# Optimization experiments

Hardware: AMD Instinct MI355X
Metric: run time of the kernel (lower is better)

The kernel has to match this reference:

```python
import jax, jax.numpy as jnp
import numpy as np

B, C, HH, WW = 16, 256, 64, 64
K, H, U, R = 16, 4, 4, 23
DIM_OUT = 256
DV = DIM_OUT // H  # 64
N = HH * WW
EPS = 1e-3  # keras BatchNormalization default epsilon


def setup_inputs() -> dict:
    key = jax.random.key(0)
    ks = jax.random.split(key, 16)
    sc = 0.02
    return {
        "x": jax.random.normal(ks[0], (B, C, HH, WW), jnp.float32),
        "w_q": jax.random.normal(ks[1], (K * H, C), jnp.float32) * sc,
        "w_k": jax.random.normal(ks[2], (K * U, C), jnp.float32) * sc,
        "w_v": jax.random.normal(ks[3], (DV * U, C), jnp.float32) * sc,
        "gamma_q": jnp.ones((K * H,), jnp.float32),
        "beta_q": jnp.zeros((K * H,), jnp.float32),
        "mean_q": jax.random.normal(ks[4], (K * H,), jnp.float32) * 0.1,
        "var_q": jax.random.uniform(ks[5], (K * H,), jnp.float32) + 0.5,
        "gamma_v": jnp.ones((DV * U,), jnp.float32),
        "beta_v": jnp.zeros((DV * U,), jnp.float32),
        "mean_v": jax.random.normal(ks[6], (DV * U,), jnp.float32) * 0.1,
        "var_v": jax.random.uniform(ks[7], (DV * U,), jnp.float32) + 0.5,
        "w_pos": jax.random.normal(ks[8], (K, U, 1, R, R), jnp.float32) * sc,
        "b_pos": jnp.zeros((K,), jnp.float32),
    }


def _bn(x, gamma, beta, mean, var):
    # inference-mode batchnorm over channel axis 1, x: [b,c,h,w]
    inv = gamma * jax.lax.rsqrt(var + EPS)
    return x * inv[None, :, None, None] + (beta - mean * inv)[None, :, None, None]


def reference(x, w_q, w_k, w_v, gamma_q, beta_q, mean_q, var_q,
              gamma_v, beta_v, mean_v, var_v, w_pos, b_pos):
    b = x.shape[0]
    # 1x1 conv projections (channels-first)
    q = jnp.einsum('oc,bchw->bohw', w_q, x)
    k = jnp.einsum('oc,bchw->bohw', w_k, x)
    v = jnp.einsum('oc,bchw->bohw', w_v, x)
    q = _bn(q, gamma_q, beta_q, mean_q, var_q)
    v = _bn(v, gamma_v, beta_v, mean_v, var_v)
    # rearrange to sequence form
    q = q.reshape(b, H, K, N)           # b h k n
    k = k.reshape(b, U, K, N)           # b u k m
    v = v.reshape(b, U, DV, N)          # b u v m
    k = jax.nn.softmax(k, axis=-1)      # softmax over positions m
    # content lambda
    Lc = jnp.einsum('bukm,buvm->bkv', k, v)
    Yc = jnp.einsum('bhkn,bkv->bnhv', q, Lc)
    # position lambda via local 3D conv over (v, hh, ww) with kernel (1, r, r)
    v5 = v.reshape(b, U, DV, HH, WW)
    Lp = jax.lax.conv_general_dilated(
        v5, w_pos, window_strides=(1, 1, 1),
        padding=[(0, 0), (R // 2, R // 2), (R // 2, R // 2)],
        dimension_numbers=('NCDHW', 'OIDHW', 'NCDHW'))
    Lp = Lp + b_pos[None, :, None, None, None]
    Lp = Lp.reshape(b, K, DV, N)        # b k v n
    Yp = jnp.einsum('bhkn,bkvn->bnhv', q, Lp)
    Y = Yc + Yp                          # [b, n, h, v]
    out = Y.transpose(0, 2, 3, 1).reshape(b, H * DV, HH, WW)
    return out
```

## Files before the change

### kernel.cpp

```cpp
#include <hip/hip_runtime.h>
#include <stdint.h>

#define EPS 1e-3f

typedef _Float16 f16x8 __attribute__((ext_vector_type(8)));
typedef float f32x4 __attribute__((ext_vector_type(4)));
typedef float f32x16 __attribute__((ext_vector_type(16)));

__global__ __launch_bounds__(256) void setup_kernel(
    const float* __restrict__ w_pos,
    const float* __restrict__ w_q, const float* __restrict__ w_k,
    const float* __restrict__ w_v,
    const float* __restrict__ gq, const float* __restrict__ bq,
    const float* __restrict__ mq, const float* __restrict__ vq,
    const float* __restrict__ gv, const float* __restrict__ bv,
    const float* __restrict__ mv, const float* __restrict__ vvar,
    float* __restrict__ scale_bias, float* __restrict__ Lc,
    _Float16* __restrict__ Wp, _Float16* __restrict__ Apack) {
  const int idx = blockIdx.x * 256 + threadIdx.x;
  if (idx < 384) {
    float sc, bi;
    if (idx < 64) {
      const float inv = gq[idx] * rsqrtf(vq[idx] + EPS);
      sc = inv; bi = bq[idx] - mq[idx] * inv;
    } else if (idx < 128) {
      sc = 1.f; bi = 0.f;
    } else {
      const int o = idx - 128;
      const float inv = gv[o] * rsqrtf(vvar[o] + EPS);
      sc = inv; bi = bv[o] - mv[o] * inv;
    }
    scale_bias[idx] = sc;
    scale_bias[384 + idx] = bi;
  }
  if (idx < 16384) Lc[idx] = 0.f;
  if (idx < 98304) {
    const int j = idx & 7;
    const int lane = (idx >> 3) & 63;
    const int fr = idx >> 9;
    const int kt = fr & 15;
    const int mt = fr >> 4;
    const int m = mt * 32 + (lane & 31);
    const int k = kt * 16 + (lane >> 5) * 8 + j;
    float sc; const float* Wsrc;
    if (m < 64) {
      sc = gq[m] * rsqrtf(vq[m] + EPS);
      Wsrc = w_q + (size_t)m * 256;
    } else if (m < 128) {
      sc = 1.f;
      Wsrc = w_k + (size_t)(m - 64) * 256;
    } else {
      const int r = m - 128;
      sc = gv[r] * rsqrtf(vvar[r] + EPS);
      Wsrc = w_v + (size_t)r * 256;
    }
    Wp[idx] = (_Float16)(Wsrc[k] * sc);
  }
  if (idx < 376832) {
    const int j = idx & 7;
    const int lane = (idx >> 3) & 63;
    const int f = idx >> 9;
    const int rel = f & 7;
    const int ss = (f >> 3) % 23;
    const int w = (f >> 3) / 23;
    const int m = lane & 31;
    const int kk = m & 15;
    const int ol = m >> 4;
    const int kap = lane >> 5;
    const int k = kap * 8 + j;
    const int u = k >> 2;
    const int y4 = k & 3;
    const int dy = 4 * rel + y4 - 2 * w - ol;
    float val = 0.f;
    if (dy >= 0 && dy < 23)
      val = w_pos[kk * 2116 + u * 529 + dy * 23 + ss];
    Apack[idx] = (_Float16)val;
  }
}

__global__ __launch_bounds__(256) void proj_gemm(
    const float* __restrict__ x, const _Float16* __restrict__ Wp,
    const float* __restrict__ scale_bias, float* __restrict__ proj) {
  const int b = blockIdx.y;
  const int n0 = blockIdx.x * 32;
  const int tid = threadIdx.x;
  const int w = tid >> 6, lane = tid & 63;
  const int col = lane & 31, kap = lane >> 5;

  __shared__ __align__(16) _Float16 xT[32][264];

#pragma unroll
  for (int r = 0; r < 8; ++r) {
    const int i = tid + r * 256;
    const int k = i >> 3, n4 = (i & 7) * 4;
    const float4 xv = *(const float4*)&x[((size_t)(b * 256 + k)) * 4096 + n0 + n4];
    xT[n4 + 0][k] = (_Float16)xv.x;
    xT[n4 + 1][k] = (_Float16)xv.y;
    xT[n4 + 2][k] = (_Float16)xv.z;
    xT[n4 + 3][k] = (_Float16)xv.w;
  }
  __syncthreads();

  f32x16 acc[3];
#pragma unroll
  for (int i = 0; i < 3; ++i) acc[i] = (f32x16)0.f;

  const f16x8* Wf = (const f16x8*)Wp;
#pragma unroll
  for (int kt = 0; kt < 16; ++kt) {
    const f16x8 B =
        *(const f16x8*)__builtin_assume_aligned(&xT[col][kt * 16 + kap * 8], 16);
#pragma unroll
    for (int i = 0; i < 3; ++i) {
      const f16x8 A = Wf[(size_t)(((w * 3 + i) * 16 + kt) * 64) + lane];
      acc[i] = __builtin_amdgcn_mfma_f32_32x32x16_f16(A, B, acc[i], 0, 0, 0);
    }
  }

#pragma unroll
  for (int i = 0; i < 3; ++i) {
    const int mt = w * 3 + i;
#pragma unroll
    for (int reg = 0; reg < 16; ++reg) {
      const int row = (reg & 3) + 8 * (reg >> 2) + 4 * kap;
      const int o = mt * 32 + row;
      proj[((size_t)(b * 384 + o)) * 4096 + n0 + col] =
          acc[i][reg] + scale_bias[384 + o];
    }
  }
}

__global__ __launch_bounds__(256) void kstats_kernel(
    const float* __restrict__ proj, float* __restrict__ kstat) {
  const int row = blockIdx.x;
  const int b = row >> 6, c = row & 63;
  const float* p = proj + ((size_t)(b * 384 + 64 + c)) * 4096;
  const int tid = threadIdx.x;

  float4 v[4];
  float vmax = -3.4e38f;
#pragma unroll
  for (int i = 0; i < 4; i++) {
    v[i] = ((const float4*)p)[tid + i * 256];
    vmax = fmaxf(vmax, fmaxf(fmaxf(v[i].x, v[i].y), fmaxf(v[i].z, v[i].w)));
  }
#pragma unroll
  for (int off = 32; off > 0; off >>= 1) vmax = fmaxf(vmax, __shfl_xor(vmax, off));
  __shared__ float redm[4], reds[4];
  if ((tid & 63) == 0) redm[tid >> 6] = vmax;
  __syncthreads();
  vmax = fmaxf(fmaxf(redm[0], redm[1]), fmaxf(redm[2], redm[3]));

  float sum = 0.f;
#pragma unroll
  for (int i = 0; i < 4; i++) {
    sum += expf(v[i].x - vmax) + expf(v[i].y - vmax) +
           expf(v[i].z - vmax) + expf(v[i].w - vmax);
  }
#pragma unroll
  for (int off = 32; off > 0; off >>= 1) sum += __shfl_xor(sum, off);
  if ((tid & 63) == 0) reds[tid >> 6] = sum;
  __syncthreads();
  sum = reds[0] + reds[1] + reds[2] + reds[3];
  if (tid == 0) {
    kstat[(size_t)row * 2 + 0] = vmax;
    kstat[(size_t)row * 2 + 1] = 1.f / sum;
  }
}

__global__ __launch_bounds__(256) void lc_kernel(const float* __restrict__ proj,
                                                 const float* __restrict__ kstat,
                                                 float* __restrict__ Lc) {
  const int mc = blockIdx.x, b = blockIdx.y;
  const int m0 = mc * 128;
  const int tid = threadIdx.x;
  const int kk = tid & 15;
  const int dvb = tid >> 4;

  __shared__ float kT[16][132];
  __shared__ float vT[64][132];

  float a0 = 0.f, a1 = 0.f, a2 = 0.f, a3 = 0.f;

  for (int u = 0; u < 4; ++u) {
    __syncthreads();
#pragma unroll
    for (int r = 0; r < 2; ++r) {
      const int i = tid + r * 256;
      const int row = i >> 5, c4 = (i & 31) * 4;
      const int ch = u * 16 + row;
      const float kmax = kstat[((size_t)b * 64 + ch) * 2 + 0];
      const float kinv = kstat[((size_t)b * 64 + ch) * 2 + 1];
      const float4 raw =
          *(const float4*)&proj[((size_t)(b * 384 + 64 + ch)) * 4096 + m0 + c4];
      float4 sm;
      sm.x = expf(raw.x - kmax) * kinv;
      sm.y = expf(raw.y - kmax) * kinv;
      sm.z = expf(raw.z - kmax) * kinv;
      sm.w = expf(raw.w - kmax) * kinv;
      *(float4*)&kT[row][c4] = sm;
    }
#pragma unroll
    for (int r = 0; r < 8; ++r) {
      const int i = tid + r * 256;
      const int row = i >> 5, c4 = (i & 31) * 4;
      *(float4*)&vT[row][c4] =
          *(const float4*)&proj[((size_t)(b * 384 + 128 + u * 64 + row)) * 4096 + m0 + c4];
    }
    __syncthreads();
#pragma unroll 4
    for (int m = 0; m < 128; ++m) {
      const float kv = kT[kk][m];
      a0 = fmaf(kv, vT[dvb * 4 + 0][m], a0);
      a1 = fmaf(kv, vT[dvb * 4 + 1][m], a1);
      a2 = fmaf(kv, vT[dvb * 4 + 2][m], a2);
      a3 = fmaf(kv, vT[dvb * 4 + 3][m], a3);
    }
  }

  float* dst = &Lc[((size_t)(b * 16 + kk)) * 64 + dvb * 4];
  atomicAdd(dst + 0, a0);
  atomicAdd(dst + 1, a1);
  atomicAdd(dst + 2, a2);
  atomicAdd(dst + 3, a3);
}

template <int W>
__device__ __forceinline__ void conv_worker(
    const _Float16* __restrict__ vL, const f16x8* __restrict__ Awl,
    const float* __restrict__ qsec, const float* __restrict__ lcb,
    const int n, const int kap, const int b, const int dv,
    float* __restrict__ out) {
  constexpr bool G0 = (W < 2);
  constexpr bool G6 = (W != 0);
  constexpr bool G7 = (W == 3);

  f16x8 A[8];
  if (G0) A[0] = Awl[0 * 64];
#pragma unroll
  for (int r = 1; r < 6; ++r) A[r] = Awl[r * 64];
  if (G6) A[6] = Awl[6 * 64];
  if (G7) A[7] = Awl[7 * 64];

#pragma unroll 1
  for (int pass = 0; pass < 2; ++pass) {
    f32x16 acc[8];
#pragma unroll
    for (int t = 0; t < 8; t++) acc[t] = (f32x16)0.f;

#pragma unroll 1
    for (int ss = 0; ss < 23; ++ss) {
      const int ssn = (ss == 22) ? 0 : ss + 1;
      const f16x8* Awn = Awl + (size_t)(ssn * 8) * 64;
      const _Float16* brow = &vL[(32 * pass + n + ss) * 360 + 8 * kap];

      f16x8 Bq[22];
      if (G0) Bq[0] = *(const f16x8*)__builtin_assume_aligned(brow, 16);
#pragma unroll
      for (int tau = 1; tau < 4; ++tau)
        Bq[tau] = *(const f16x8*)__builtin_assume_aligned(brow + 16 * tau, 16);

#pragma unroll
      for (int tau = 0; tau < 22; ++tau) {
        const int tpf = tau + 4;
        if (tpf < 22) {
          const bool live = (tpf == 20) ? G6 : (tpf == 21) ? G7 : true;
          if (live)
            Bq[tpf] = *(const f16x8*)__builtin_assume_aligned(brow + 16 * tpf, 16);
        }
        __builtin_amdgcn_s_setprio(1);
#pragma unroll
        for (int t = 0; t < 8; ++t) {
          const int rel = tau - 2 * t;
          if (rel < 0 || rel > 7) continue;
          if ((rel == 0 && !G0) || (rel == 6 && !G6) || (rel == 7 && !G7)) continue;
          acc[t] = __builtin_amdgcn_mfma_f32_32x32x16_f16(A[rel], Bq[tau], acc[t], 0, 0, 0);
        }
        __builtin_amdgcn_s_setprio(0);
        if (tau >= 14) {
          const int rn = tau - 14;
          const bool live = (rn == 0) ? G0 : (rn == 6) ? G6 : (rn == 7) ? G7 : true;
          if (live) A[rn] = Awn[rn * 64];
        }
      }
    }

    const int c = 32 * pass + n;
#pragma unroll 1
    for (int t = 0; t < 8; ++t) {
#pragma unroll
      for (int ol = 0; ol < 2; ++ol) {
        const int gamma = 8 * t + 2 * W + ol;
        const float* qg = qsec + (size_t)gamma * 64 + c;
        float y0 = 0.f, y1 = 0.f, y2 = 0.f, y3 = 0.f;
#pragma unroll
        for (int e = 0; e < 8; ++e) {
          const int kk = (e & 3) + 8 * (e >> 2) + 4 * kap;
          const float cf = acc[t][ol * 8 + e] + lcb[e];
          y0 = fmaf(qg[(size_t)(kk) * 4096], cf, y0);
          y1 = fmaf(qg[(size_t)(16 + kk) * 4096], cf, y1);
          y2 = fmaf(qg[(size_t)(32 + kk) * 4096], cf, y2);
          y3 = fmaf(qg[(size_t)(48 + kk) * 4096], cf, y3);
        }
        y0 += __shfl_xor(y0, 32);
        y1 += __shfl_xor(y1, 32);
        y2 += __shfl_xor(y2, 32);
        y3 += __shfl_xor(y3, 32);
        const float s0 = kap ? y2 : y0;
        const float s1 = kap ? y3 : y1;
        out[((size_t)(b * 256 + (2 * kap + 0) * 64 + dv)) * 4096 + gamma * 64 + c] = s0;
        out[((size_t)(b * 256 + (2 * kap + 1) * 64 + dv)) * 4096 + gamma * 64 + c] = s1;
      }
    }
  }
}

__global__ __launch_bounds__(256, 2) void lambda_conv(
    const float* __restrict__ proj, const _Float16* __restrict__ Apack,
    const float* __restrict__ Lc, const float* __restrict__ b_pos,
    float* __restrict__ out) {
  const int wgid = blockIdx.x;
  const int xcd = wgid & 7;
  const int slot = wgid >> 3;
  const int b = (xcd << 1) | (slot >> 6);
  const int dv = slot & 63;
  const int tid = threadIdx.x;
  const int w = tid >> 6;
  const int lane = tid & 63;
  const int n = lane & 31;
  const int kap = lane >> 5;

  __shared__ __align__(16) _Float16 vL[86 * 360];

  {
    const uint4 z = {0u, 0u, 0u, 0u};
    for (int i = tid; i < (86 * 360 * 2) / 16; i += 256) ((uint4*)vL)[i] = z;
  }
  __syncthreads();

  {
    const float* vsec = proj + ((size_t)(b * 384 + 128 + dv)) * 4096;
    for (int idx = tid; idx < 4096; idx += 256) {
      const int u = idx >> 10, g = (idx >> 4) & 63, c4 = (idx & 15) * 4;
      const float4 vv = *(const float4*)&vsec[(size_t)u * 262144 + g * 64 + c4];
      const int sy = g + 11;
      const int qoff = (sy >> 2) * 16 + (u << 2) + (sy & 3);
      _Float16* base = &vL[(c4 + 11) * 360 + qoff];
      base[0 * 360] = (_Float16)vv.x;
      base[1 * 360] = (_Float16)vv.y;
      base[2 * 360] = (_Float16)vv.z;
      base[3 * 360] = (_Float16)vv.w;
    }
  }
  __syncthreads();

  float lcb[8];
#pragma unroll
  for (int e = 0; e < 8; e++) {
    const int kk = (e & 3) + 8 * (e >> 2) + 4 * kap;
    lcb[e] = Lc[(b * 16 + kk) * 64 + dv] + b_pos[kk];
  }

  const float* qsec = proj + ((size_t)(b * 384)) * 4096;
  const f16x8* Ap = (const f16x8*)Apack;
  const f16x8* Awl = Ap + (size_t)(w * 184) * 64 + lane;

  switch (w) {
    case 0: conv_worker<0>(vL, Awl, qsec, lcb, n, kap, b, dv, out); break;
    case 1: conv_worker<1>(vL, Awl, qsec, lcb, n, kap, b, dv, out); break;
    case 2: conv_worker<2>(vL, Awl, qsec, lcb, n, kap, b, dv, out); break;
    default: conv_worker<3>(vL, Awl, qsec, lcb, n, kap, b, dv, out); break;
  }
}

extern "C" void kernel_launch(void* const* d_in, const int* in_sizes, int n_in,
                              void* d_out, int out_size, void* d_ws, size_t ws_size,
                              hipStream_t stream) {
  const float* x       = (const float*)d_in[0];
  const float* w_q     = (const float*)d_in[1];
  const float* w_k     = (const float*)d_in[2];
  const float* w_v     = (const float*)d_in[3];
  const float* gamma_q = (const float*)d_in[4];
  const float* beta_q  = (const float*)d_in[5];
  const float* mean_q  = (const float*)d_in[6];
  const float* var_q   = (const float*)d_in[7];
  const float* gamma_v = (const float*)d_in[8];
  const float* beta_v  = (const float*)d_in[9];
  const float* mean_v  = (const float*)d_in[10];
  const float* var_v   = (const float*)d_in[11];
  const float* w_pos   = (const float*)d_in[12];
  const float* b_pos   = (const float*)d_in[13];

  float* ws = (float*)d_ws;
  float* proj = ws;
  float* sb   = ws + 25165824;
  float* Lc   = sb + 768;
  _Float16* Apack = (_Float16*)(Lc + 16384);
  _Float16* Wp = Apack + 376832;
  float* kstat = (float*)(Wp + 98304);
  float* out = (float*)d_out;

  setup_kernel<<<1472, 256, 0, stream>>>(w_pos, w_q, w_k, w_v,
                                         gamma_q, beta_q, mean_q, var_q,
                                         gamma_v, beta_v, mean_v, var_v,
                                         sb, Lc, Wp, Apack);
  proj_gemm<<<dim3(128, 16), 256, 0, stream>>>(x, Wp, sb, proj);
  kstats_kernel<<<1024, 256, 0, stream>>>(proj, kstat);
  lc_kernel<<<dim3(32, 16), 256, 0, stream>>>(proj, kstat, Lc);
  lambda_conv<<<1024, 256, 0, stream>>>(proj, Apack, Lc, b_pos, out);
}
```

Before: 519.8 us.

## Store key/value projections as fp16 and drop XCD-aware block mapping

The projection GEMM now writes the query projection in fp32 to its own buffer and the key and value projections in fp16 to a separate buffer. The k-statistics, content-lambda and positional-conv kernels read 8-wide fp16 vectors instead of fp32. This roughly halves the global traffic for the largest intermediate. The lambda_conv launch also changes from an XCD-swizzled 1D grid to a plain 2D (dv, b) grid, which may change L2 locality. The softmax max and sum are now taken over fp16-rounded keys, adding a small precision loss.

```diff
diff --git a/kernel.cpp b/kernel.cpp
--- a/kernel.cpp
+++ b/kernel.cpp
@@ -80,7 +80,8 @@
 
 __global__ __launch_bounds__(256) void proj_gemm(
     const float* __restrict__ x, const _Float16* __restrict__ Wp,
-    const float* __restrict__ scale_bias, float* __restrict__ proj) {
+    const float* __restrict__ scale_bias, float* __restrict__ projq,
+    _Float16* __restrict__ projkv) {
   const int b = blockIdx.y;
   const int n0 = blockIdx.x * 32;
   const int tid = threadIdx.x;
@@ -124,26 +125,30 @@
     for (int reg = 0; reg < 16; ++reg) {
       const int row = (reg & 3) + 8 * (reg >> 2) + 4 * kap;
       const int o = mt * 32 + row;
-      proj[((size_t)(b * 384 + o)) * 4096 + n0 + col] =
-          acc[i][reg] + scale_bias[384 + o];
+      const float val = acc[i][reg] + scale_bias[384 + o];
+      if (mt < 2)
+        projq[((size_t)(b * 64 + o)) * 4096 + n0 + col] = val;
+      else
+        projkv[((size_t)(b * 320 + (o - 64))) * 4096 + n0 + col] = (_Float16)val;
     }
   }
 }
 
 __global__ __launch_bounds__(256) void kstats_kernel(
-    const float* __restrict__ proj, float* __restrict__ kstat) {
+    const _Float16* __restrict__ projkv, float* __restrict__ kstat) {
   const int row = blockIdx.x;
   const int b = row >> 6, c = row & 63;
-  const float* p = proj + ((size_t)(b * 384 + 64 + c)) * 4096;
+  const f16x8* p8 = (const f16x8*)(projkv + ((size_t)(b * 320 + c)) * 4096);
   const int tid = threadIdx.x;
 
-  float4 v[4];
+  f16x8 h[2];
+  h[0] = p8[tid];
+  h[1] = p8[tid + 256];
   float vmax = -3.4e38f;
 #pragma unroll
-  for (int i = 0; i < 4; i++) {
-    v[i] = ((const float4*)p)[tid + i * 256];
-    vmax = fmaxf(vmax, fmaxf(fmaxf(v[i].x, v[i].y), fmaxf(v[i].z, v[i].w)));
-  }
+  for (int i = 0; i < 2; ++i)
+#pragma unroll
+    for (int e = 0; e < 8; ++e) vmax = fmaxf(vmax, (float)h[i][e]);
 #pragma unroll
   for (int off = 32; off > 0; off >>= 1) vmax = fmaxf(vmax, __shfl_xor(vmax, off));
   __shared__ float redm[4], reds[4];
@@ -153,10 +158,9 @@
 
   float sum = 0.f;
 #pragma unroll
-  for (int i = 0; i < 4; i++) {
-    sum += expf(v[i].x - vmax) + expf(v[i].y - vmax) +
-           expf(v[i].z - vmax) + expf(v[i].w - vmax);
-  }
+  for (int i = 0; i < 2; ++i)
+#pragma unroll
+    for (int e = 0; e < 8; ++e) sum += expf((float)h[i][e] - vmax);
 #pragma unroll
   for (int off = 32; off > 0; off >>= 1) sum += __shfl_xor(sum, off);
   if ((tid & 63) == 0) reds[tid >> 6] = sum;
@@ -168,9 +172,9 @@
   }
 }
 
-__global__ __launch_bounds__(256) void lc_kernel(const float* __restrict__ proj,
-                                                 const float* __restrict__ kstat,
-                                                 float* __restrict__ Lc) {
+__global__ __launch_bounds__(256) void lc_kernel(
+    const _Float16* __restrict__ projkv, const float* __restrict__ kstat,
+    float* __restrict__ Lc) {
   const int mc = blockIdx.x, b = blockIdx.y;
   const int m0 = mc * 128;
   const int tid = threadIdx.x;
@@ -184,28 +188,25 @@
 
   for (int u = 0; u < 4; ++u) {
     __syncthreads();
-#pragma unroll
-    for (int r = 0; r < 2; ++r) {
-      const int i = tid + r * 256;
-      const int row = i >> 5, c4 = (i & 31) * 4;
+    {
+      const int row = tid >> 4, c8 = (tid & 15) * 8;
       const int ch = u * 16 + row;
       const float kmax = kstat[((size_t)b * 64 + ch) * 2 + 0];
       const float kinv = kstat[((size_t)b * 64 + ch) * 2 + 1];
-      const float4 raw =
-          *(const float4*)&proj[((size_t)(b * 384 + 64 + ch)) * 4096 + m0 + c4];
-      float4 sm;
-      sm.x = expf(raw.x - kmax) * kinv;
-      sm.y = expf(raw.y - kmax) * kinv;
-      sm.z = expf(raw.z - kmax) * kinv;
-      sm.w = expf(raw.w - kmax) * kinv;
-      *(float4*)&kT[row][c4] = sm;
-    }
-#pragma unroll
-    for (int r = 0; r < 8; ++r) {
+      const f16x8 raw =
+          *(const f16x8*)&projkv[((size_t)(b * 320 + ch)) * 4096 + m0 + c8];
+#pragma unroll
+      for (int e = 0; e < 8; ++e)
+        kT[row][c8 + e] = expf((float)raw[e] - kmax) * kinv;
+    }
+#pragma unroll
+    for (int r = 0; r < 4; ++r) {
       const int i = tid + r * 256;
-      const int row = i >> 5, c4 = (i & 31) * 4;
-      *(float4*)&vT[row][c4] =
-          *(const float4*)&proj[((size_t)(b * 384 + 128 + u * 64 + row)) * 4096 + m0 + c4];
+      const int row = i >> 4, c8 = (i & 15) * 8;
+      const f16x8 raw =
+          *(const f16x8*)&projkv[((size_t)(b * 320 + 64 + u * 64 + row)) * 4096 + m0 + c8];
+#pragma unroll
+      for (int e = 0; e < 8; ++e) vT[row][c8 + e] = (float)raw[e];
     }
     __syncthreads();
 #pragma unroll 4
@@ -316,14 +317,12 @@
 }
 
 __global__ __launch_bounds__(256, 2) void lambda_conv(
-    const float* __restrict__ proj, const _Float16* __restrict__ Apack,
+    const float* __restrict__ projq, const _Float16* __restrict__ projkv,
+    const _Float16* __restrict__ Apack,
     const float* __restrict__ Lc, const float* __restrict__ b_pos,
     float* __restrict__ out) {
-  const int wgid = blockIdx.x;
-  const int xcd = wgid & 7;
-  const int slot = wgid >> 3;
-  const int b = (xcd << 1) | (slot >> 6);
-  const int dv = slot & 63;
+  const int dv = blockIdx.x;
+  const int b = blockIdx.y;
   const int tid = threadIdx.x;
   const int w = tid >> 6;
   const int lane = tid & 63;
@@ -339,17 +338,15 @@
   __syncthreads();
 
   {
-    const float* vsec = proj + ((size_t)(b * 384 + 128 + dv)) * 4096;
-    for (int idx = tid; idx < 4096; idx += 256) {
-      const int u = idx >> 10, g = (idx >> 4) & 63, c4 = (idx & 15) * 4;
-      const float4 vv = *(const float4*)&vsec[(size_t)u * 262144 + g * 64 + c4];
+    const _Float16* vsec = projkv + ((size_t)(b * 320 + 64 + dv)) * 4096;
+    for (int idx = tid; idx < 2048; idx += 256) {
+      const int u = idx >> 9, g = (idx >> 3) & 63, c8 = (idx & 7) * 8;
+      const f16x8 vv = *(const f16x8*)&vsec[(size_t)u * 262144 + g * 64 + c8];
       const int sy = g + 11;
       const int qoff = (sy >> 2) * 16 + (u << 2) + (sy & 3);
-      _Float16* base = &vL[(c4 + 11) * 360 + qoff];
-      base[0 * 360] = (_Float16)vv.x;
-      base[1 * 360] = (_Float16)vv.y;
-      base[2 * 360] = (_Float16)vv.z;
-      base[3 * 360] = (_Float16)vv.w;
+      _Float16* base = &vL[(c8 + 11) * 360 + qoff];
+#pragma unroll
+      for (int e = 0; e < 8; ++e) base[(size_t)e * 360] = vv[e];
     }
   }
   __syncthreads();
@@ -361,7 +358,7 @@
     lcb[e] = Lc[(b * 16 + kk) * 64 + dv] + b_pos[kk];
   }
 
-  const float* qsec = proj + ((size_t)(b * 384)) * 4096;
+  const float* qsec = projq + ((size_t)(b * 64)) * 4096;
   const f16x8* Ap = (const f16x8*)Apack;
   const f16x8* Awl = Ap + (size_t)(w * 184) * 64 + lane;
 
@@ -392,9 +389,10 @@
   const float* b_pos   = (const float*)d_in[13];
 
   float* ws = (float*)d_ws;
-  float* proj = ws;
-  float* sb   = ws + 25165824;
-  float* Lc   = sb + 768;
+  float* projq = ws;
+  _Float16* projkv = (_Float16*)(ws + 4194304);
+  float* sb = ws + 4194304 + 10485760;
+  float* Lc = sb + 768;
   _Float16* Apack = (_Float16*)(Lc + 16384);
   _Float16* Wp = Apack + 376832;
   float* kstat = (float*)(Wp + 98304);
@@ -404,8 +402,8 @@
                                          gamma_q, beta_q, mean_q, var_q,
                                          gamma_v, beta_v, mean_v, var_v,
                                          sb, Lc, Wp, Apack);
-  proj_gemm<<<dim3(128, 16), 256, 0, stream>>>(x, Wp, sb, proj);
-  kstats_kernel<<<1024, 256, 0, stream>>>(proj, kstat);
-  lc_kernel<<<dim3(32, 16), 256, 0, stream>>>(proj, kstat, Lc);
-  lambda_conv<<<1024, 256, 0, stream>>>(proj, Apack, Lc, b_pos, out);
-}
+  proj_gemm<<<dim3(128, 16), 256, 0, stream>>>(x, Wp, sb, projq, projkv);
+  kstats_kernel<<<1024, 256, 0, stream>>>(projkv, kstat);
+  lc_kernel<<<dim3(32, 16), 256, 0, stream>>>(projkv, kstat, Lc);
+  lambda_conv<<<dim3(64, 16), 256, 0, stream>>>(projq, projkv, Apack, Lc, b_pos, out);
+}
```

Measured after the change: 510.3 us (median of 2 runs). About the same (-1.8%).
